# Kernel optimization log

Hardware: AMD Instinct MI355X
Metric: run time of the kernel (lower is better)

The kernel has to match this reference:

```python
import jax, jax.numpy as jnp
import numpy as np

BN_EPS = 1e-5


def _conv2d(x, w, b, pad):
    # x: [B,C,H,W], w: [O,I,kh,kw] (OIHW)
    y = jax.lax.conv_general_dilated(
        x, w, window_strides=(1, 1), padding=[(pad, pad), (pad, pad)],
        dimension_numbers=('NCHW', 'OIHW', 'NCHW'))
    return y + b[None, :, None, None]


def setup_inputs() -> dict:
    key = jax.random.key(0)
    ks = jax.random.split(key, 4)
    B, C, D, H, W = 8, 256, 1, 64, 64
    dm = 256
    x = jax.random.normal(ks[0], (B, C, D, H, W), dtype=jnp.float32)
    wq = jax.random.normal(ks[1], (dm, dm, 1, 1), dtype=jnp.float32) * 0.05
    bq = jnp.zeros((dm,), jnp.float32)
    wkv = jax.random.normal(ks[2], (2 * dm, dm, 3, 3), dtype=jnp.float32) * 0.05
    bkv = jnp.zeros((2 * dm,), jnp.float32)
    gamma = jnp.ones((dm,), jnp.float32)
    beta = jnp.zeros((dm,), jnp.float32)
    return {"x": x, "wq": wq, "bq": bq, "wkv": wkv, "bkv": bkv,
            "gamma": gamma, "beta": beta}


def reference(x, wq, bq, wkv, bkv, gamma, beta):
    B = x.shape[0]
    H, W = x.shape[-2], x.shape[-1]
    xc = x.reshape(B, -1, H, W)            # 'b c d h w -> b (c d) h w'
    dm = xc.shape[1]
    q = jax.nn.relu(_conv2d(xc, wq, bq, 0))       # [B,dm,H,W]
    kv = jax.nn.relu(_conv2d(xc, wkv, bkv, 1))    # [B,2dm,H,W]
    k, v = jnp.split(kv, 2, axis=1)

    def tok(t):  # 'b c x y -> b (x y) c'
        return t.transpose(0, 2, 3, 1).reshape(B, H * W, dm)

    qt, kt, vt = tok(q), tok(k), tok(v)
    sim = jnp.einsum('bid,bjd->bij', qt, kt)       # [B,N,N]
    A = jax.nn.softmax(sim / jnp.sqrt(jnp.float32(dm)), axis=-1)
    r = jnp.einsum('bij,bjd->bid', A, vt)          # [B,N,dm]
    r = r.reshape(B, H, W, dm).transpose(0, 3, 1, 2)  # 'b (x y) c -> b c x y'
    y = r + xc
    # BatchNorm2d, training mode: batch stats over (B,H,W), biased variance
    mean = jnp.mean(y, axis=(0, 2, 3), keepdims=True)
    var = jnp.var(y, axis=(0, 2, 3), keepdims=True)
    out = (y - mean) * jax.lax.rsqrt(var + BN_EPS)
    out = out * gamma[None, :, None, None] + beta[None, :, None, None]
    return out
```

## Files before the change

### kernel.cpp

```cpp
#include <hip/hip_runtime.h>


typedef __attribute__((ext_vector_type(8))) short bf16x8;
typedef __attribute__((ext_vector_type(4))) float f32x4;
typedef __attribute__((ext_vector_type(8))) unsigned short u16x8;

__device__ inline unsigned short f2bf(float f) {
  union { float f; unsigned u; } c; c.f = f;
  unsigned u = c.u;
  return (unsigned short)((u + 0x7fffu + ((u >> 16) & 1u)) >> 16);
}

__device__ inline unsigned cvtpk(float lo, float hi) {
  unsigned r;
  asm("v_cvt_pk_bf16_f32 %0, %1, %2" : "=v"(r) : "v"(lo), "v"(hi));
  return r;
}

__device__ inline void dma16(const void* g, void* l) {
  __builtin_amdgcn_global_load_lds(
      (const __attribute__((address_space(1))) unsigned int*)g,
      (__attribute__((address_space(3))) unsigned int*)l, 16, 0, 0);
}

__global__ __launch_bounds__(256) void k_xt(
    const float* __restrict__ x, ushort* __restrict__ xt)
{
  const int b = blockIdx.z, ci0 = blockIdx.y * 64, gx = blockIdx.x;
  const int t = threadIdx.x;
  ushort* img = xt + (size_t)b * 4224 * 256;
  if (gx >= 64) {
    int r0 = (gx == 64) ? 0 : 4160;
#pragma unroll
    for (int k = 0; k < 2; ++k) {
      int idx = t + k * 256;
      int r = idx >> 3, u = idx & 7;
      u16x8 z = (u16x8)0;
      *(u16x8*)&img[(size_t)(r0 + r) * 256 + ci0 + u * 8] = z;
    }
    return;
  }
  const int n0 = gx * 64;
  __shared__ ushort tl[64][65];
  {
    const float* xb = x + ((size_t)b * 256 + ci0) * 4096 + n0;
    int i = t >> 2, j0 = (t & 3) * 16;
#pragma unroll
    for (int jj = 0; jj < 16; jj += 4) {
      float4 v = *(const float4*)&xb[(size_t)i * 4096 + j0 + jj];
      tl[j0 + jj + 0][i] = f2bf(v.x);
      tl[j0 + jj + 1][i] = f2bf(v.y);
      tl[j0 + jj + 2][i] = f2bf(v.z);
      tl[j0 + jj + 3][i] = f2bf(v.w);
    }
  }
  __syncthreads();
  {
    int j = t >> 3, u = t & 7;
#pragma unroll
    for (int k = 0; k < 2; ++k) {
      int jr = j + k * 32;
      ushort tmp[8];
#pragma unroll
      for (int e = 0; e < 8; ++e) tmp[e] = tl[jr][u * 8 + e];
      *(u16x8*)&img[(size_t)(64 + n0 + jr) * 256 + ci0 + u * 8] = *(u16x8*)tmp;
    }
  }
}

__global__ __launch_bounds__(256) void k_wprep(
    const float* __restrict__ w, ushort* __restrict__ wt, int ntaps, int nco)
{
  const int co = blockIdx.x;
  const int t = threadIdx.x;
  __shared__ float ws[2304];
  const int tot = 256 * ntaps;
  for (int i = t; i < tot; i += 256) ws[i] = w[(size_t)co * tot + i];
  __syncthreads();
  for (int tap = 0; tap < ntaps; ++tap)
    wt[((size_t)tap * nco + co) * 256 + t] = f2bf(ws[t * ntaps + tap]);
}

__global__ __launch_bounds__(256, 2) void k_conv(
    const ushort* __restrict__ xt, const ushort* __restrict__ wt,
    const float* __restrict__ bias, ushort* __restrict__ outT,
    ushort* __restrict__ outV, int ntaps, int nco, float oscale)
{
  extern __shared__ unsigned char smem[];
  ushort* As0 = (ushort*)smem;
  ushort* As1 = (ushort*)(smem + 16512);
  ushort* Bs0 = (ushort*)(smem + 33024);
  ushort* Bs1 = (ushort*)(smem + 33024 + 16384);
  __shared__ float bias_s[256];

  const int t = threadIdx.x, lane = t & 63;
  const int wv = t >> 6, wm = wv >> 1, wn = wv & 1;
  const int qc = lane & 15, grp = lane >> 4;
  const int b = blockIdx.z, n0 = blockIdx.x * 128, co0 = blockIdx.y * 256;
  const bool nchw = (outV != nullptr) && (blockIdx.y == 1);
  const ushort* img = xt + (size_t)b * 4224 * 256 + (size_t)64 * 256;
  const int wbase = t & ~63;

  bias_s[t] = bias[co0 + t];

  f32x4 acc[4][8];
#pragma unroll
  for (int mi = 0; mi < 4; ++mi)
#pragma unroll
    for (int ni = 0; ni < 8; ++ni) acc[mi][ni] = f32x4{0.f, 0.f, 0.f, 0.f};

  auto stageA = [&](int c8, ushort* dst) {
    const int ci0 = c8 * 32;
#pragma unroll
    for (int k = 0; k < 5; ++k) {
      int idx = k * 256 + t;
      if (idx < 1032) {
        int r = idx >> 2, u = idx & 3;
        int n = min(max(n0 + r - 65, -64), 4159);
        dma16(img + (size_t)n * 256 + ci0 + u * 8,
              dst + (size_t)(k * 256 + wbase) * 8);
      }
    }
  };
  auto stageB = [&](int tap, int c8, ushort* dst) {
    const ushort* wrow = wt + ((size_t)tap * nco + co0) * 256 + c8 * 32;
#pragma unroll
    for (int k = 0; k < 4; ++k) {
      int idx = k * 256 + t;
      int r = idx >> 2, u = idx & 3;
      dma16(wrow + (size_t)r * 256 + u * 8,
            dst + (size_t)(k * 256 + wbase) * 8);
    }
  };

  stageA(0, As0);
  stageB(0, 0, Bs0);
  asm volatile("s_waitcnt vmcnt(0)" ::: "memory");
  __syncthreads();

  const int niters = 8 * ntaps;
  int iter = 0;
  for (int c8 = 0; c8 < 8; ++c8) {
    const ushort* Asb = (c8 & 1) ? As1 : As0;
    for (int tap = 0; tap < ntaps; ++tap, ++iter) {
      const ushort* Bsb = (iter & 1) ? Bs1 : Bs0;
      if (iter + 1 < niters) {
        int ntap = (tap + 1 == ntaps) ? 0 : tap + 1;
        int nc8  = (tap + 1 == ntaps) ? c8 + 1 : c8;
        stageB(ntap, nc8, (iter & 1) ? Bs0 : Bs1);
        if (ntap == 0) stageA(nc8, (c8 & 1) ? As0 : As1);
      }
      const int dy = (ntaps == 9) ? (tap / 3 - 1) : 0;
      const int dx = (ntaps == 9) ? (tap % 3 - 1) : 0;
      const int off = dy * 64 + dx;
      bf16x8 bf[8];
#pragma unroll
      for (int ni = 0; ni < 8; ++ni)
        bf[ni] = *(const bf16x8*)&Bsb[(wn * 128 + ni * 16 + qc) * 32 + grp * 8];
#pragma unroll
      for (int mi = 0; mi < 4; ++mi) {
        int ar = wm * 64 + mi * 16 + qc + off + 65;
        bf16x8 af = *(const bf16x8*)&Asb[ar * 32 + grp * 8];
        if (dx < 0 && mi == 0 && qc == 0)  af = (bf16x8)0;
        if (dx > 0 && mi == 3 && qc == 15) af = (bf16x8)0;
#pragma unroll
        for (int ni = 0; ni < 8; ++ni)
          acc[mi][ni] = __builtin_amdgcn_mfma_f32_16x16x32_bf16(af, bf[ni], acc[mi][ni], 0, 0, 0);
      }
      asm volatile("s_waitcnt vmcnt(0)" ::: "memory");
      __syncthreads();
    }
  }

  if (!nchw) {
    ushort (*olds)[264] = (ushort(*)[264])smem;
#pragma unroll
    for (int mi = 0; mi < 4; ++mi) {
      int p = wm * 64 + mi * 16 + grp * 4;
#pragma unroll
      for (int ni = 0; ni < 8; ++ni) {
        int c = wn * 128 + ni * 16 + qc;
        float bv = bias_s[c];
#pragma unroll
        for (int r = 0; r < 4; ++r)
          olds[p + r][c] = f2bf(fmaxf(acc[mi][ni][r] + bv, 0.f) * oscale);
      }
    }
    __syncthreads();
    ushort* dst = outT + ((size_t)b * 4096 + n0) * 256;
#pragma unroll
    for (int k = 0; k < 16; ++k) {
      int idx = t + k * 256;
      int r = idx >> 5, u = idx & 31;
      *(u16x8*)&dst[(size_t)r * 256 + u * 8] = *(const u16x8*)&olds[r][u * 8];
    }
  } else {
    ushort (*oldsT)[136] = (ushort(*)[136])smem;
#pragma unroll
    for (int mi = 0; mi < 4; ++mi) {
      int p = wm * 64 + mi * 16 + grp * 4;
#pragma unroll
      for (int ni = 0; ni < 8; ++ni) {
        int c = wn * 128 + ni * 16 + qc;
        float bv = bias_s[c];
        ushort4 pk;
        pk.x = f2bf(fmaxf(acc[mi][ni][0] + bv, 0.f) * oscale);
        pk.y = f2bf(fmaxf(acc[mi][ni][1] + bv, 0.f) * oscale);
        pk.z = f2bf(fmaxf(acc[mi][ni][2] + bv, 0.f) * oscale);
        pk.w = f2bf(fmaxf(acc[mi][ni][3] + bv, 0.f) * oscale);
        *(ushort4*)&oldsT[c][p] = pk;
      }
    }
    __syncthreads();
    ushort* dst = outV + (size_t)b * 256 * 4096 + n0;
#pragma unroll
    for (int k = 0; k < 16; ++k) {
      int idx = t + k * 256;
      int c = idx >> 4, u = idx & 15;
      *(u16x8*)&dst[(size_t)c * 4096 + u * 8] = *(const u16x8*)&oldsT[c][u * 8];
    }
  }
}

__global__ __launch_bounds__(512, 2) void k_attn(
    const ushort* __restrict__ q_t, const ushort* __restrict__ k_t,
    const ushort* __restrict__ v_t, const float* __restrict__ x,
    float* __restrict__ y, float* __restrict__ gstat)
{
  extern __shared__ unsigned char smem[];
  ushort* kbf0 = (ushort*)smem;
  ushort* kbf1 = (ushort*)(smem + 32768);
  ushort* vbf0 = (ushort*)(smem + 65536);
  ushort* vbf1 = (ushort*)(smem + 98304);
  ushort* pl   = (ushort*)(smem + 131072);

  const int tid = threadIdx.x, lane = tid & 63, w = tid >> 6;
  const int grp = lane >> 4, qc = lane & 15, xr = qc & 7;
  const int b = blockIdx.y, q0 = blockIdx.x * 128;
  const int wbase = tid & ~63;

  int offk[4], offv[4];
#pragma unroll
  for (int k = 0; k < 4; ++k) {
    int i = k * 512 + tid;
    int j = i >> 5, s = i & 31;
    offk[k] = j * 256 + ((s ^ (j & 7)) << 3);
    int d = i >> 3, s2 = i & 7;
    offv[k] = d * 4096 + ((s2 ^ (d & 7)) << 3);
  }
  const ushort* kT = k_t + (size_t)b * 4096 * 256;
  const ushort* vT = v_t + (size_t)b * 256 * 4096;

  bf16x8 qf[8];
  {
    const ushort* qrow = q_t + ((size_t)b * 4096 + q0 + w * 16 + qc) * 256;
#pragma unroll
    for (int dc = 0; dc < 8; ++dc)
      qf[dc] = *(const bf16x8*)&qrow[dc * 32 + grp * 8];
  }

  f32x4 o[16];
#pragma unroll
  for (int dt = 0; dt < 16; ++dt) o[dt] = f32x4{0.f, 0.f, 0.f, 0.f};
  float m_run = -1e30f, lp = 0.f;

  auto stage = [&](const ushort* kp, const ushort* vp, ushort* kb, ushort* vb) {
#pragma unroll
    for (int k = 0; k < 4; ++k)
      dma16(kp + offk[k], kb + (size_t)(k * 512 + wbase) * 8);
#pragma unroll
    for (int k = 0; k < 4; ++k)
      dma16(vp + offv[k], vb + (size_t)(k * 512 + wbase) * 8);
  };

  stage(kT, vT, kbf0, vbf0);
  kT += 16384; vT += 64;
  asm volatile("s_waitcnt vmcnt(0)" ::: "memory");
  __syncthreads();

  ushort* prow = pl + (size_t)(w * 16 + qc) * 64;
  int po[4], pslot[2];
#pragma unroll
  for (int kt = 0; kt < 4; ++kt)
    po[kt] = (((2 * kt + (grp >> 1)) ^ xr) << 3) + ((grp & 1) << 2);
#pragma unroll
  for (int kc = 0; kc < 2; ++kc)
    pslot[kc] = ((kc * 4 + grp) ^ xr) << 3;

  for (int t = 0; t < 64; ++t) {
    ushort* kb = (t & 1) ? kbf1 : kbf0;
    ushort* vb = (t & 1) ? vbf1 : vbf0;
    if (t < 63) {
      stage(kT, vT, (t & 1) ? kbf0 : kbf1, (t & 1) ? vbf0 : vbf1);
      kT += 16384; vT += 64;
    }

    f32x4 st[4];
    __builtin_amdgcn_s_setprio(1);
#pragma unroll
    for (int kt = 0; kt < 4; ++kt) {
      const int row = (kt * 16 + qc) * 256;
      bf16x8 ka8[8];
#pragma unroll
      for (int dc = 0; dc < 8; ++dc)
        ka8[dc] = *(const bf16x8*)&kb[row + (((dc * 4 + grp) ^ xr) << 3)];
      f32x4 a = f32x4{0.f, 0.f, 0.f, 0.f};
#pragma unroll
      for (int dc = 0; dc < 8; ++dc)
        a = __builtin_amdgcn_mfma_f32_16x16x32_bf16(ka8[dc], qf[dc], a, 0, 0, 0);
      st[kt] = a;
    }
    __builtin_amdgcn_s_setprio(0);

    float pmax = fmaxf(
        fmaxf(fmaxf(st[0][0], st[0][1]), fmaxf(st[0][2], st[0][3])),
        fmaxf(fmaxf(st[1][0], st[1][1]), fmaxf(st[1][2], st[1][3])));
    pmax = fmaxf(pmax, fmaxf(
        fmaxf(fmaxf(st[2][0], st[2][1]), fmaxf(st[2][2], st[2][3])),
        fmaxf(fmaxf(st[3][0], st[3][1]), fmaxf(st[3][2], st[3][3]))));
    pmax = fmaxf(pmax, __shfl_xor(pmax, 16));
    pmax = fmaxf(pmax, __shfl_xor(pmax, 32));
    if (pmax - m_run > 11.5f) {
      float mn = fmaxf(m_run, pmax);
      float al = exp2f(m_run - mn);
      m_run = mn; lp *= al;
#pragma unroll
      for (int dt = 0; dt < 16; ++dt) {
        o[dt][0] *= al; o[dt][1] *= al; o[dt][2] *= al; o[dt][3] *= al;
      }
    }
#pragma unroll
    for (int kt = 0; kt < 4; ++kt) {
      float p0 = exp2f(st[kt][0] - m_run);
      float p1 = exp2f(st[kt][1] - m_run);
      float p2 = exp2f(st[kt][2] - m_run);
      float p3 = exp2f(st[kt][3] - m_run);
      lp += (p0 + p1) + (p2 + p3);
      uint2 pk = { cvtpk(p0, p1), cvtpk(p2, p3) };
      *(uint2*)&prow[po[kt]] = pk;
    }

    bf16x8 pb0 = *(const bf16x8*)&prow[pslot[0]];
    bf16x8 pb1 = *(const bf16x8*)&prow[pslot[1]];
    bf16x8 vaA[8], vaB[8];
#pragma unroll
    for (int j = 0; j < 8; ++j) {
      int dt = j >> 1;
      vaA[j] = *(const bf16x8*)&vb[(dt * 16 + qc) * 64 + pslot[j & 1]];
    }
    __builtin_amdgcn_s_setprio(1);
#pragma unroll
    for (int bt = 0; bt < 4; ++bt) {
      const bf16x8* cur = (bt & 1) ? vaB : vaA;
      bf16x8* nxt = (bt & 1) ? vaA : vaB;
      if (bt < 3) {
#pragma unroll
        for (int j = 0; j < 8; ++j) {
          int dt = (bt + 1) * 4 + (j >> 1);
          nxt[j] = *(const bf16x8*)&vb[(dt * 16 + qc) * 64 + pslot[j & 1]];
        }
      }
#pragma unroll
      for (int j2 = 0; j2 < 4; ++j2) {
        int dt = bt * 4 + j2;
        o[dt] = __builtin_amdgcn_mfma_f32_16x16x32_bf16(cur[2 * j2],     pb0, o[dt], 0, 0, 0);
        o[dt] = __builtin_amdgcn_mfma_f32_16x16x32_bf16(cur[2 * j2 + 1], pb1, o[dt], 0, 0, 0);
      }
    }
    __builtin_amdgcn_s_setprio(0);

    asm volatile("s_waitcnt vmcnt(0)" ::: "memory");
    __syncthreads();
  }

  lp += __shfl_xor(lp, 16);
  lp += __shfl_xor(lp, 32);
  float inv = 1.f / lp;

  float (*obuf)[132] = (float(*)[132])smem;
  float* part1 = (float*)(smem + 135168);
  float* part2 = (float*)(smem + 136192);
#pragma unroll
  for (int dt = 0; dt < 16; ++dt)
#pragma unroll
    for (int r = 0; r < 4; ++r)
      obuf[dt * 16 + grp * 4 + r][w * 16 + qc] = o[dt][r] * inv;
  __syncthreads();

  const float* xb = x + (size_t)b * 256 * 4096 + q0;
  float*       yb = y + (size_t)b * 256 * 4096 + q0;
#pragma unroll
  for (int k = 0; k < 16; ++k) {
    int i = tid + k * 512;
    int c = i >> 5, f4 = (i & 31) << 2;
    float4 xr4 = *(const float4*)&xb[(size_t)c * 4096 + f4];
    float4 rv = *(const float4*)&obuf[c][f4];
    rv.x += xr4.x; rv.y += xr4.y; rv.z += xr4.z; rv.w += xr4.w;
    *(float4*)&yb[(size_t)c * 4096 + f4] = rv;
    float ls1 = (rv.x + rv.y) + (rv.z + rv.w);
    float ls2 = (rv.x * rv.x + rv.y * rv.y) + (rv.z * rv.z + rv.w * rv.w);
#pragma unroll
    for (int sh = 1; sh <= 16; sh <<= 1) {
      ls1 += __shfl_xor(ls1, sh);
      ls2 += __shfl_xor(ls2, sh);
    }
    if ((tid & 31) == 0) { part1[c] = ls1; part2[c] = ls2; }
  }
  __syncthreads();
  if (tid < 256) {
    atomicAdd(&gstat[tid], part1[tid]);
    atomicAdd(&gstat[256 + tid], part2[tid]);
  }
}

__global__ __launch_bounds__(256) void k_bnapply(
    float* __restrict__ y, const float* __restrict__ gstat,
    const float* __restrict__ gamma, const float* __restrict__ beta)
{
  __shared__ float sc_s[256], sh_s[256];
  {
    const int c = threadIdx.x;
    float mean = gstat[c] * (1.f / 32768.f);
    float var  = gstat[256 + c] * (1.f / 32768.f) - mean * mean;
    float inv  = rsqrtf(var + 1e-5f);
    float g = gamma[c] * inv;
    sc_s[c] = g;
    sh_s[c] = beta[c] - mean * g;
  }
  __syncthreads();
  const int total4 = 8 * 256 * 1024;
  for (int i = blockIdx.x * 256 + threadIdx.x; i < total4; i += gridDim.x * 256) {
    int c = (i >> 10) & 255;
    float sc = sc_s[c], sh = sh_s[c];
    float4 v = ((const float4*)y)[i];
    v.x = fmaf(v.x, sc, sh);
    v.y = fmaf(v.y, sc, sh);
    v.z = fmaf(v.z, sc, sh);
    v.w = fmaf(v.w, sc, sh);
    ((float4*)y)[i] = v;
  }
}

extern "C" void kernel_launch(void* const* d_in, const int* in_sizes, int n_in,
                              void* d_out, int out_size, void* d_ws, size_t ws_size,
                              hipStream_t stream) {
  const float* x     = (const float*)d_in[0];
  const float* wq    = (const float*)d_in[1];
  const float* bq    = (const float*)d_in[2];
  const float* wkv   = (const float*)d_in[3];
  const float* bkv   = (const float*)d_in[4];
  const float* gamma = (const float*)d_in[5];
  const float* beta  = (const float*)d_in[6];
  float* out = (float*)d_out;

  ushort* xt  = (ushort*)d_ws;
  ushort* wt3 = xt  + (size_t)8650752;
  ushort* wt1 = wt3 + (size_t)1179648;
  ushort* q_t = wt1 + (size_t)65536;
  ushort* k_t = q_t + (size_t)8388608;
  ushort* v_t = k_t + (size_t)8388608;
  float* gstat = (float*)(v_t + (size_t)8388608);

  hipMemsetAsync(gstat, 0, 2048, stream);

  k_xt<<<dim3(66, 4, 8), 256, 0, stream>>>(x, xt);
  k_wprep<<<dim3(512), 256, 0, stream>>>(wkv, wt3, 9, 512);
  k_wprep<<<dim3(256), 256, 0, stream>>>(wq, wt1, 1, 256);

  const int conv_smem = 69632;
  hipFuncSetAttribute(reinterpret_cast<const void*>(k_conv),
                      hipFuncAttributeMaxDynamicSharedMemorySize, conv_smem);
  k_conv<<<dim3(32, 1, 8), 256, conv_smem, stream>>>(
      xt, wt1, bq, q_t, nullptr, 1, 256, 0.0625f * 1.44269504f);
  k_conv<<<dim3(32, 2, 8), 256, conv_smem, stream>>>(
      xt, wt3, bkv, k_t, v_t, 9, 512, 1.0f);

  const int attn_smem = 147456;
  hipFuncSetAttribute(reinterpret_cast<const void*>(k_attn),
                      hipFuncAttributeMaxDynamicSharedMemorySize, attn_smem);
  k_attn<<<dim3(32, 8), 512, attn_smem, stream>>>(q_t, k_t, v_t, x, out, gstat);

  k_bnapply<<<dim3(2048), 256, 0, stream>>>(out, gstat, gamma, beta);
}
```

Before: 292.8 us.

## Switch attention to 32x32x16 MFMA with in-register P via permlane32 swap

Rewrites the attention inner loop to use 32x32x16 bf16 MFMA tiles, so each wave handles 32 queries against 64 keys and the block shrinks to 4 waves of 256 threads. The softmax probabilities are repacked into the B-operand layout with v_permlane32_swap instead of a round trip through an LDS buffer, which removes the P staging stores and loads. The intent is fewer LDS operations and fewer, larger MFMAs per tile. In exchange there is lower wave parallelism per block, more accumulator registers per thread, and twice as many DMA issues per thread.

After: 328.6 us. 12.2% more time.

```diff
diff --git a/kernel.cpp b/kernel.cpp
--- a/kernel.cpp
+++ b/kernel.cpp
@@ -3,6 +3,7 @@
 
 typedef __attribute__((ext_vector_type(8))) short bf16x8;
 typedef __attribute__((ext_vector_type(4))) float f32x4;
+typedef __attribute__((ext_vector_type(16))) float f32x16;
 typedef __attribute__((ext_vector_type(8))) unsigned short u16x8;
 
 __device__ inline unsigned short f2bf(float f) {
@@ -222,7 +223,7 @@
   }
 }
 
-__global__ __launch_bounds__(512, 2) void k_attn(
+__global__ __launch_bounds__(256, 1) void k_attn(
     const ushort* __restrict__ q_t, const ushort* __restrict__ k_t,
     const ushort* __restrict__ v_t, const float* __restrict__ x,
     float* __restrict__ y, float* __restrict__ gstat)
@@ -232,17 +233,16 @@
   ushort* kbf1 = (ushort*)(smem + 32768);
   ushort* vbf0 = (ushort*)(smem + 65536);
   ushort* vbf1 = (ushort*)(smem + 98304);
-  ushort* pl   = (ushort*)(smem + 131072);
 
   const int tid = threadIdx.x, lane = tid & 63, w = tid >> 6;
-  const int grp = lane >> 4, qc = lane & 15, xr = qc & 7;
+  const int q32 = lane & 31, gK = lane >> 5, swz = lane & 7;
   const int b = blockIdx.y, q0 = blockIdx.x * 128;
   const int wbase = tid & ~63;
 
-  int offk[4], offv[4];
-#pragma unroll
-  for (int k = 0; k < 4; ++k) {
-    int i = k * 512 + tid;
+  int offk[8], offv[8];
+#pragma unroll
+  for (int k = 0; k < 8; ++k) {
+    int i = k * 256 + tid;
     int j = i >> 5, s = i & 31;
     offk[k] = j * 256 + ((s ^ (j & 7)) << 3);
     int d = i >> 3, s2 = i & 7;
@@ -251,26 +251,27 @@
   const ushort* kT = k_t + (size_t)b * 4096 * 256;
   const ushort* vT = v_t + (size_t)b * 256 * 4096;
 
-  bf16x8 qf[8];
+  bf16x8 qf[16];
   {
-    const ushort* qrow = q_t + ((size_t)b * 4096 + q0 + w * 16 + qc) * 256;
-#pragma unroll
-    for (int dc = 0; dc < 8; ++dc)
-      qf[dc] = *(const bf16x8*)&qrow[dc * 32 + grp * 8];
-  }
-
-  f32x4 o[16];
-#pragma unroll
-  for (int dt = 0; dt < 16; ++dt) o[dt] = f32x4{0.f, 0.f, 0.f, 0.f};
+    const ushort* qrow =
+        q_t + ((size_t)b * 4096 + q0 + w * 32 + q32) * 256 + gK * 8;
+#pragma unroll
+    for (int ds = 0; ds < 16; ++ds)
+      qf[ds] = *(const bf16x8*)&qrow[ds * 16];
+  }
+
+  f32x16 o[8];
+#pragma unroll
+  for (int db = 0; db < 8; ++db) o[db] = (f32x16)0.f;
   float m_run = -1e30f, lp = 0.f;
 
   auto stage = [&](const ushort* kp, const ushort* vp, ushort* kb, ushort* vb) {
 #pragma unroll
-    for (int k = 0; k < 4; ++k)
-      dma16(kp + offk[k], kb + (size_t)(k * 512 + wbase) * 8);
-#pragma unroll
-    for (int k = 0; k < 4; ++k)
-      dma16(vp + offv[k], vb + (size_t)(k * 512 + wbase) * 8);
+    for (int k = 0; k < 8; ++k)
+      dma16(kp + offk[k], kb + (size_t)(k * 256 + wbase) * 8);
+#pragma unroll
+    for (int k = 0; k < 8; ++k)
+      dma16(vp + offv[k], vb + (size_t)(k * 256 + wbase) * 8);
   };
 
   stage(kT, vT, kbf0, vbf0);
@@ -278,14 +279,12 @@
   asm volatile("s_waitcnt vmcnt(0)" ::: "memory");
   __syncthreads();
 
-  ushort* prow = pl + (size_t)(w * 16 + qc) * 64;
-  int po[4], pslot[2];
-#pragma unroll
-  for (int kt = 0; kt < 4; ++kt)
-    po[kt] = (((2 * kt + (grp >> 1)) ^ xr) << 3) + ((grp & 1) << 2);
-#pragma unroll
-  for (int kc = 0; kc < 2; ++kc)
-    pslot[kc] = ((kc * 4 + grp) ^ xr) << 3;
+  int kcol[16], vcol[4];
+#pragma unroll
+  for (int ds = 0; ds < 16; ++ds) kcol[ds] = ((2 * ds + gK) ^ swz) << 3;
+#pragma unroll
+  for (int ks = 0; ks < 4; ++ks) vcol[ks] = ((2 * ks + gK) ^ swz) << 3;
+  const int krow0 = q32 * 256, krow1 = (q32 + 32) * 256;
 
   for (int t = 0; t < 64; ++t) {
     ushort* kb = (t & 1) ? kbf1 : kbf0;
@@ -295,76 +294,81 @@
       kT += 16384; vT += 64;
     }
 
-    f32x4 st[4];
+    f32x16 s0 = (f32x16)0.f, s1 = (f32x16)0.f;
     __builtin_amdgcn_s_setprio(1);
 #pragma unroll
-    for (int kt = 0; kt < 4; ++kt) {
-      const int row = (kt * 16 + qc) * 256;
-      bf16x8 ka8[8];
-#pragma unroll
-      for (int dc = 0; dc < 8; ++dc)
-        ka8[dc] = *(const bf16x8*)&kb[row + (((dc * 4 + grp) ^ xr) << 3)];
-      f32x4 a = f32x4{0.f, 0.f, 0.f, 0.f};
-#pragma unroll
-      for (int dc = 0; dc < 8; ++dc)
-        a = __builtin_amdgcn_mfma_f32_16x16x32_bf16(ka8[dc], qf[dc], a, 0, 0, 0);
-      st[kt] = a;
+    for (int ds = 0; ds < 16; ++ds) {
+      bf16x8 a0 = *(const bf16x8*)&kb[krow0 + kcol[ds]];
+      bf16x8 a1 = *(const bf16x8*)&kb[krow1 + kcol[ds]];
+      s0 = __builtin_amdgcn_mfma_f32_32x32x16_bf16(a0, qf[ds], s0, 0, 0, 0);
+      s1 = __builtin_amdgcn_mfma_f32_32x32x16_bf16(a1, qf[ds], s1, 0, 0, 0);
     }
     __builtin_amdgcn_s_setprio(0);
 
-    float pmax = fmaxf(
-        fmaxf(fmaxf(st[0][0], st[0][1]), fmaxf(st[0][2], st[0][3])),
-        fmaxf(fmaxf(st[1][0], st[1][1]), fmaxf(st[1][2], st[1][3])));
-    pmax = fmaxf(pmax, fmaxf(
-        fmaxf(fmaxf(st[2][0], st[2][1]), fmaxf(st[2][2], st[2][3])),
-        fmaxf(fmaxf(st[3][0], st[3][1]), fmaxf(st[3][2], st[3][3]))));
-    pmax = fmaxf(pmax, __shfl_xor(pmax, 16));
+    float pmax;
+    {
+      float m0 = fmaxf(fmaxf(s0[0], s0[1]), fmaxf(s0[2], s0[3]));
+      m0 = fmaxf(m0, fmaxf(fmaxf(s0[4], s0[5]), fmaxf(s0[6], s0[7])));
+      m0 = fmaxf(m0, fmaxf(fmaxf(s0[8], s0[9]), fmaxf(s0[10], s0[11])));
+      m0 = fmaxf(m0, fmaxf(fmaxf(s0[12], s0[13]), fmaxf(s0[14], s0[15])));
+      float m1 = fmaxf(fmaxf(s1[0], s1[1]), fmaxf(s1[2], s1[3]));
+      m1 = fmaxf(m1, fmaxf(fmaxf(s1[4], s1[5]), fmaxf(s1[6], s1[7])));
+      m1 = fmaxf(m1, fmaxf(fmaxf(s1[8], s1[9]), fmaxf(s1[10], s1[11])));
+      m1 = fmaxf(m1, fmaxf(fmaxf(s1[12], s1[13]), fmaxf(s1[14], s1[15])));
+      pmax = fmaxf(m0, m1);
+    }
     pmax = fmaxf(pmax, __shfl_xor(pmax, 32));
     if (pmax - m_run > 11.5f) {
       float mn = fmaxf(m_run, pmax);
       float al = exp2f(m_run - mn);
       m_run = mn; lp *= al;
 #pragma unroll
-      for (int dt = 0; dt < 16; ++dt) {
-        o[dt][0] *= al; o[dt][1] *= al; o[dt][2] *= al; o[dt][3] *= al;
-      }
-    }
-#pragma unroll
-    for (int kt = 0; kt < 4; ++kt) {
-      float p0 = exp2f(st[kt][0] - m_run);
-      float p1 = exp2f(st[kt][1] - m_run);
-      float p2 = exp2f(st[kt][2] - m_run);
-      float p3 = exp2f(st[kt][3] - m_run);
-      lp += (p0 + p1) + (p2 + p3);
-      uint2 pk = { cvtpk(p0, p1), cvtpk(p2, p3) };
-      *(uint2*)&prow[po[kt]] = pk;
-    }
-
-    bf16x8 pb0 = *(const bf16x8*)&prow[pslot[0]];
-    bf16x8 pb1 = *(const bf16x8*)&prow[pslot[1]];
-    bf16x8 vaA[8], vaB[8];
-#pragma unroll
-    for (int j = 0; j < 8; ++j) {
-      int dt = j >> 1;
-      vaA[j] = *(const bf16x8*)&vb[(dt * 16 + qc) * 64 + pslot[j & 1]];
-    }
+      for (int db = 0; db < 8; ++db) o[db] *= al;
+    }
+    float p0[16], p1[16];
+#pragma unroll
+    for (int r = 0; r < 16; ++r) {
+      p0[r] = exp2f(s0[r] - m_run);
+      p1[r] = exp2f(s1[r] - m_run);
+      lp += p0[r] + p1[r];
+    }
+
+    bf16x8 pB[4];
+    {
+      unsigned a0 = cvtpk(p0[0], p0[1]),  a1 = cvtpk(p0[2], p0[3]);
+      unsigned a2 = cvtpk(p0[4], p0[5]),  a3 = cvtpk(p0[6], p0[7]);
+      unsigned a4 = cvtpk(p0[8], p0[9]),  a5 = cvtpk(p0[10], p0[11]);
+      unsigned a6 = cvtpk(p0[12], p0[13]), a7 = cvtpk(p0[14], p0[15]);
+      asm volatile("v_permlane32_swap_b32 %0, %1" : "+v"(a0), "+v"(a2));
+      asm volatile("v_permlane32_swap_b32 %0, %1" : "+v"(a1), "+v"(a3));
+      asm volatile("v_permlane32_swap_b32 %0, %1" : "+v"(a4), "+v"(a6));
+      asm volatile("v_permlane32_swap_b32 %0, %1" : "+v"(a5), "+v"(a7));
+      union { unsigned u[4]; bf16x8 v; } f0, f1;
+      f0.u[0] = a0; f0.u[1] = a1; f0.u[2] = a2; f0.u[3] = a3;
+      f1.u[0] = a4; f1.u[1] = a5; f1.u[2] = a6; f1.u[3] = a7;
+      pB[0] = f0.v; pB[1] = f1.v;
+      unsigned b0 = cvtpk(p1[0], p1[1]),  b1 = cvtpk(p1[2], p1[3]);
+      unsigned b2 = cvtpk(p1[4], p1[5]),  b3 = cvtpk(p1[6], p1[7]);
+      unsigned b4 = cvtpk(p1[8], p1[9]),  b5 = cvtpk(p1[10], p1[11]);
+      unsigned b6 = cvtpk(p1[12], p1[13]), b7 = cvtpk(p1[14], p1[15]);
+      asm volatile("v_permlane32_swap_b32 %0, %1" : "+v"(b0), "+v"(b2));
+      asm volatile("v_permlane32_swap_b32 %0, %1" : "+v"(b1), "+v"(b3));
+      asm volatile("v_permlane32_swap_b32 %0, %1" : "+v"(b4), "+v"(b6));
+      asm volatile("v_permlane32_swap_b32 %0, %1" : "+v"(b5), "+v"(b7));
+      union { unsigned u[4]; bf16x8 v; } f2, f3;
+      f2.u[0] = b0; f2.u[1] = b1; f2.u[2] = b2; f2.u[3] = b3;
+      f3.u[0] = b4; f3.u[1] = b5; f3.u[2] = b6; f3.u[3] = b7;
+      pB[2] = f2.v; pB[3] = f3.v;
+    }
+
     __builtin_amdgcn_s_setprio(1);
 #pragma unroll
-    for (int bt = 0; bt < 4; ++bt) {
-      const bf16x8* cur = (bt & 1) ? vaB : vaA;
-      bf16x8* nxt = (bt & 1) ? vaA : vaB;
-      if (bt < 3) {
-#pragma unroll
-        for (int j = 0; j < 8; ++j) {
-          int dt = (bt + 1) * 4 + (j >> 1);
-          nxt[j] = *(const bf16x8*)&vb[(dt * 16 + qc) * 64 + pslot[j & 1]];
-        }
-      }
-#pragma unroll
-      for (int j2 = 0; j2 < 4; ++j2) {
-        int dt = bt * 4 + j2;
-        o[dt] = __builtin_amdgcn_mfma_f32_16x16x32_bf16(cur[2 * j2],     pb0, o[dt], 0, 0, 0);
-        o[dt] = __builtin_amdgcn_mfma_f32_16x16x32_bf16(cur[2 * j2 + 1], pb1, o[dt], 0, 0, 0);
+    for (int db = 0; db < 8; ++db) {
+      const int vbase = (db * 32 + q32) * 64;
+#pragma unroll
+      for (int ks = 0; ks < 4; ++ks) {
+        bf16x8 va = *(const bf16x8*)&vb[vbase + vcol[ks]];
+        o[db] = __builtin_amdgcn_mfma_f32_32x32x16_bf16(va, pB[ks], o[db], 0, 0, 0);
       }
     }
     __builtin_amdgcn_s_setprio(0);
@@ -373,7 +377,6 @@
     __syncthreads();
   }
 
-  lp += __shfl_xor(lp, 16);
   lp += __shfl_xor(lp, 32);
   float inv = 1.f / lp;
 
@@ -381,17 +384,19 @@
   float* part1 = (float*)(smem + 135168);
   float* part2 = (float*)(smem + 136192);
 #pragma unroll
-  for (int dt = 0; dt < 16; ++dt)
-#pragma unroll
-    for (int r = 0; r < 4; ++r)
-      obuf[dt * 16 + grp * 4 + r][w * 16 + qc] = o[dt][r] * inv;
+  for (int db = 0; db < 8; ++db)
+#pragma unroll
+    for (int r = 0; r < 16; ++r) {
+      int d = db * 32 + (r & 3) + 8 * (r >> 2) + 4 * gK;
+      obuf[d][w * 32 + q32] = o[db][r] * inv;
+    }
   __syncthreads();
 
   const float* xb = x + (size_t)b * 256 * 4096 + q0;
   float*       yb = y + (size_t)b * 256 * 4096 + q0;
 #pragma unroll
-  for (int k = 0; k < 16; ++k) {
-    int i = tid + k * 512;
+  for (int k = 0; k < 32; ++k) {
+    int i = tid + k * 256;
     int c = i >> 5, f4 = (i & 31) << 2;
     float4 xr4 = *(const float4*)&xb[(size_t)c * 4096 + f4];
     float4 rv = *(const float4*)&obuf[c][f4];
@@ -407,10 +412,8 @@
     if ((tid & 31) == 0) { part1[c] = ls1; part2[c] = ls2; }
   }
   __syncthreads();
-  if (tid < 256) {
-    atomicAdd(&gstat[tid], part1[tid]);
-    atomicAdd(&gstat[256 + tid], part2[tid]);
-  }
+  atomicAdd(&gstat[tid], part1[tid]);
+  atomicAdd(&gstat[256 + tid], part2[tid]);
 }
 
 __global__ __launch_bounds__(256) void k_bnapply(
@@ -478,7 +481,7 @@
   const int attn_smem = 147456;
   hipFuncSetAttribute(reinterpret_cast<const void*>(k_attn),
                       hipFuncAttributeMaxDynamicSharedMemorySize, attn_smem);
-  k_attn<<<dim3(32, 8), 512, attn_smem, stream>>>(q_t, k_t, v_t, x, out, gstat);
+  k_attn<<<dim3(32, 8), 256, attn_smem, stream>>>(q_t, k_t, v_t, x, out, gstat);
 
   k_bnapply<<<dim3(2048), 256, 0, stream>>>(out, gstat, gamma, beta);
 }
```
